# Kernel optimization log

Hardware: AMD Instinct MI355X
Metric: run time of the kernel (lower is better)

Reference implementation:

```python
import jax, jax.numpy as jnp
from jax import lax
import numpy as np

SEQ, BATCH, X_DIM = 256, 64, 64
FEAT = 256      # dense_x[-1]
DEC = 256       # dense_h_x[-1]
H = 512         # dim_rnn


def setup_inputs() -> dict:
    key = jax.random.key(0)
    ks = jax.random.split(key, 12)
    s = 0.05
    return {
        "x": jax.random.normal(ks[0], (SEQ, BATCH, X_DIM), jnp.float32),
        "mode_selector": jax.random.uniform(ks[1], (SEQ,), jnp.float32),
        # feature extractor: Linear(x_dim -> FEAT) + tanh
        "W_fx": jax.random.normal(ks[2], (FEAT, X_DIM), jnp.float32) * s,
        "b_fx": jnp.zeros((FEAT,), jnp.float32),
        # LSTM (single layer): gates ordered i, f, g, o (torch convention)
        "W_ih": jax.random.normal(ks[3], (4 * H, FEAT), jnp.float32) * s,
        "W_hh": jax.random.normal(ks[4], (4 * H, H), jnp.float32) * s,
        "b_ih": jnp.zeros((4 * H,), jnp.float32),
        "b_hh": jnp.zeros((4 * H,), jnp.float32),
        # decoder MLP: Linear(H -> DEC) + tanh
        "W_hx": jax.random.normal(ks[5], (DEC, H), jnp.float32) * s,
        "b_hx": jnp.zeros((DEC,), jnp.float32),
        # gen_out: Linear(DEC -> x_dim)
        "W_out": jax.random.normal(ks[6], (X_DIM, DEC), jnp.float32) * s,
        "b_out": jnp.zeros((X_DIM,), jnp.float32),
    }


def _forward(x, mode_selector, W_fx, b_fx, W_ih, W_hh, b_ih, b_hh,
             W_hx, b_hx, W_out, b_out):
    def fe(v):  # feature_extractor_x (dropout_p=0 -> identity)
        return jnp.tanh(v @ W_fx.T + b_fx)

    def gen(h):  # mlp_h_x + gen_out
        return jnp.tanh(h @ W_hx.T + b_hx) @ W_out.T + b_out

    def lstm_cell(feat, h, c):
        g = feat @ W_ih.T + b_ih + h @ W_hh.T + b_hh  # [B, 4H]
        i, f, gg, o = jnp.split(g, 4, axis=-1)
        c2 = jax.nn.sigmoid(f) * c + jax.nn.sigmoid(i) * jnp.tanh(gg)
        h2 = jax.nn.sigmoid(o) * jnp.tanh(c2)
        return h2, c2

    S, B, _ = x.shape
    feat_x = fe(x)  # [S, B, FEAT] teacher-forced features
    h0 = jnp.zeros((B, H), x.dtype)
    c0 = jnp.zeros((B, H), x.dtype)
    y0 = jnp.zeros((B, W_out.shape[0]), x.dtype)

    def step(carry, inp):
        h, c, y_prev = carry
        feat_tf, mix, is_first = inp
        # at t=0 original uses feature_x[0] as the "auto" feature
        feat_auto = jnp.where(is_first, feat_tf, fe(y_prev))
        feat = mix * feat_auto + (1.0 - mix) * feat_tf
        y_t = gen(h)           # generated from pre-update hidden state
        h2, c2 = lstm_cell(feat, h, c)
        return (h2, c2, y_t), y_t

    is_first = (jnp.arange(S) == 0)
    _, y = lax.scan(step, (h0, c0, y0), (feat_x, mode_selector, is_first))
    return y  # [S, B, x_dim]


def reference(x, mode_selector, W_fx, b_fx, W_ih, W_hh, b_ih, b_hh,
              W_hx, b_hx, W_out, b_out):
    return _forward(x, mode_selector, W_fx, b_fx, W_ih, W_hh, b_ih, b_hh,
                    W_hx, b_hx, W_out, b_out)
```

## Files before the change

### kernel.cpp

```cpp
#include <hip/hip_runtime.h>
#include <stdint.h>

typedef unsigned short u16;
typedef unsigned int u32;
typedef unsigned long long u64;
typedef __attribute__((ext_vector_type(8))) short short8;
typedef __attribute__((ext_vector_type(4))) float f32x4;
typedef __attribute__((ext_vector_type(4))) int int4v;

#define SEQ 256
#define GATE_WGS 64
#define D_WGS 8
#define NWG 73
#define A_ELE 49152
#define D_ELE 16384
#define FACC_ELE 16384

__device__ __forceinline__ u16 f2bf(float f) {
  u32 u = __float_as_uint(f);
  u += 0x7FFFu + ((u >> 16) & 1u);
  return (u16)(u >> 16);
}
__device__ __forceinline__ float bf2f(u16 v) {
  return __uint_as_float(((u32)v) << 16);
}
__device__ __forceinline__ short8 cvt8(const float* __restrict__ p) {
  short8 r;
#pragma unroll
  for (int j = 0; j < 8; ++j) r[j] = (short)f2bf(p[j]);
  return r;
}
__device__ __forceinline__ short8 cvt8v(const float* __restrict__ p) {
  f32x4 a = *(const f32x4*)p, b = *(const f32x4*)(p + 4);
  short8 r;
#pragma unroll
  for (int j = 0; j < 4; ++j) { r[j] = (short)f2bf(a[j]); r[4 + j] = (short)f2bf(b[j]); }
  return r;
}
__device__ __forceinline__ float fast_tanh(float x) {
  return 1.0f - 2.0f / (1.0f + __expf(2.0f * x));
}
__device__ __forceinline__ float fast_sig(float x) {
  return 1.0f / (1.0f + __expf(-x));
}

union V16 { short8 s; u64 q[2]; };
__device__ __forceinline__ short8 ldc16(const u16* p) {
  V16 v;
  v.q[0] = __hip_atomic_load((const u64*)p,     __ATOMIC_RELAXED, __HIP_MEMORY_SCOPE_AGENT);
  v.q[1] = __hip_atomic_load((const u64*)p + 1, __ATOMIC_RELAXED, __HIP_MEMORY_SCOPE_AGENT);
  return v.s;
}
__device__ __forceinline__ f32x4 ldc16f(const float* p) {
  union { f32x4 f; u64 q[2]; } v;
  v.q[0] = __hip_atomic_load((const u64*)p,     __ATOMIC_RELAXED, __HIP_MEMORY_SCOPE_AGENT);
  v.q[1] = __hip_atomic_load((const u64*)p + 1, __ATOMIC_RELAXED, __HIP_MEMORY_SCOPE_AGENT);
  return v.f;
}
__device__ __forceinline__ void stc16(u16* p, const u64* s) {
  __hip_atomic_store((u64*)p,     s[0], __ATOMIC_RELAXED, __HIP_MEMORY_SCOPE_AGENT);
  __hip_atomic_store((u64*)p + 1, s[1], __ATOMIC_RELAXED, __HIP_MEMORY_SCOPE_AGENT);
}
__device__ __forceinline__ void atadd(float* p, float v) {
  (void)__hip_atomic_fetch_add(p, v, __ATOMIC_RELAXED, __HIP_MEMORY_SCOPE_AGENT);
}
__device__ __forceinline__ void pollge(u32* p, u32 v) {
  while (__hip_atomic_load(p, __ATOMIC_RELAXED, __HIP_MEMORY_SCOPE_AGENT) < v) {}
}
__device__ __forceinline__ void setflag(u32* p, u32 v) {
  __hip_atomic_store(p, v, __ATOMIC_RELAXED, __HIP_MEMORY_SCOPE_AGENT);
}
#define VMCNT0() asm volatile("s_waitcnt vmcnt(0)" ::: "memory")

__global__ void prep_misc(const float* __restrict__ W_fx, const float* __restrict__ b_fx,
                          const float* __restrict__ W_out, const float* __restrict__ b_out,
                          u16* __restrict__ Abuf0, u32* __restrict__ flags,
                          float* __restrict__ featacc, float* __restrict__ bcomb,
                          u16* __restrict__ Wcpack) {
  int b = blockIdx.x, tid = threadIdx.x;
  if (b == 0) {
    for (int it = 0; it < 16; ++it) {
      int chunk = it * 256 + tid;
      *(int4v*)(Abuf0 + (2048 + chunk) * 8) = (int4v){0, 0, 0, 0};
    }
  } else if (b == 1) {
    for (int k = 0; k < 6; ++k) flags[k * 256 + tid] = 0u;
  } else if (b < 6) {
    float* base = featacc + (b - 2) * 16384;
    for (int it = 0; it < 16; ++it)
      *(f32x4*)(base + (it * 256 + tid) * 4) = (f32x4){0.f, 0.f, 0.f, 0.f};
  } else if (b == 6) {
    float s = b_fx[tid];
    for (int k = 0; k < 64; ++k) s += W_fx[tid * 64 + k] * b_out[k];
    bcomb[tid] = s;
  } else {
    int ct = b - 7;
    for (int it = 0; it < 16; ++it) {
      int o = it * 256 + tid;
      int cl = o >> 8, dec = o & 255;
      int c = ct * 16 + cl;
      float s = 0.f;
      for (int k = 0; k < 64; ++k) s += W_fx[c * 64 + k] * W_out[k * 256 + dec];
      int dw = dec >> 5, kd = dec & 31;
      int l = (c & 15) + ((kd >> 3) << 4), j = kd & 7;
      Wcpack[((dw * 16 + (c >> 4)) * 64 + l) * 8 + j] = f2bf(s);
    }
  }
}

__global__ void prep_ftf(const float* __restrict__ x, const float* __restrict__ W_fx,
                         const float* __restrict__ b_fx, u16* __restrict__ ftf) {
  __shared__ __attribute__((aligned(16))) u16 fstage[64 * 264];
  const int t = blockIdx.x, tid = threadIdx.x;
  const int wv = tid >> 6, ln = tid & 63;
  const int c15 = ln & 15, qq = ln >> 4;
  short8 WfR[2][4];
#pragma unroll
  for (int kk = 0; kk < 2; ++kk)
#pragma unroll
    for (int nt = 0; nt < 4; ++nt)
      WfR[kk][nt] = cvt8(W_fx + ((wv * 4 + nt) * 16 + c15) * 64 + kk * 32 + qq * 8);
  float bfx_r[4];
#pragma unroll
  for (int nt = 0; nt < 4; ++nt) bfx_r[nt] = b_fx[(wv * 4 + nt) * 16 + c15];
  short8 xa[2][4];
#pragma unroll
  for (int kb = 0; kb < 2; ++kb)
#pragma unroll
    for (int mt = 0; mt < 4; ++mt)
      xa[kb][mt] = cvt8v(x + (t * 64 + mt * 16 + c15) * 64 + kb * 32 + qq * 8);
  f32x4 tf[4][4];
#pragma unroll
  for (int nt = 0; nt < 4; ++nt)
#pragma unroll
    for (int mt = 0; mt < 4; ++mt) tf[nt][mt] = (f32x4){0.f, 0.f, 0.f, 0.f};
#pragma unroll
  for (int kb = 0; kb < 2; ++kb)
#pragma unroll
    for (int nt = 0; nt < 4; ++nt)
#pragma unroll
      for (int mt = 0; mt < 4; ++mt)
        tf[nt][mt] = __builtin_amdgcn_mfma_f32_16x16x32_bf16(xa[kb][mt], WfR[kb][nt], tf[nt][mt], 0, 0, 0);
#pragma unroll
  for (int nt = 0; nt < 4; ++nt)
#pragma unroll
    for (int mt = 0; mt < 4; ++mt)
#pragma unroll
      for (int r2 = 0; r2 < 4; ++r2) {
        int row = mt * 16 + qq * 4 + r2;
        fstage[row * 264 + (wv * 4 + nt) * 16 + c15] = f2bf(fast_tanh(tf[nt][mt][r2] + bfx_r[nt]));
      }
  __syncthreads();
  u16* ftfb = ftf + t * 16384;
#pragma unroll
  for (int it = 0; it < 8; ++it) {
    int chunk = it * 256 + tid;
    int kb = chunk >> 8, l = chunk & 63;
    int m = ((chunk >> 6) & 3) * 16 + (l & 15);
    int k = kb * 32 + (l >> 4) * 8;
    *(short8*)(ftfb + chunk * 8) = *(const short8*)(fstage + m * 264 + k);
  }
}

__global__ void __launch_bounds__(256, 1)
rnn_kernel(const float* __restrict__ x, const float* __restrict__ msel,
           const float* __restrict__ W_ih, const float* __restrict__ W_hh,
           const float* __restrict__ b_ih, const float* __restrict__ b_hh,
           const float* __restrict__ W_hx, const float* __restrict__ b_hx,
           const float* __restrict__ W_out, const float* __restrict__ b_out,
           float* __restrict__ out,
           u16* __restrict__ Abase, u16* __restrict__ dbase,
           u32* __restrict__ flags, float* __restrict__ featacc,
           const float* __restrict__ bcomb, const u16* __restrict__ Wcpack,
           const u16* __restrict__ ftf) {
  __shared__ __attribute__((aligned(16))) char smem[109568];
  const int wgid = blockIdx.x;
  const int tid = threadIdx.x;
  const int wv = tid >> 6, ln = tid & 63;
  u32* dflag = flags + 1024;
  u32* hcnt  = flags + 1168;
  u32* fcnt  = flags + 1232;

  if (wgid < GATE_WGS) {
    const int wg = wgid;
    float* red = (float*)smem;
    u16* hstage = (u16*)(smem + 32768);
    short8 Breg[6][2];
#pragma unroll
    for (int kk = 0; kk < 6; ++kk) {
      int kb = wv + kk * 4;
#pragma unroll
      for (int nt = 0; nt < 2; ++nt) {
        int n = ln & 15, q = ln >> 4;
        int gate = nt * 2 + (n >> 3), unit = n & 7;
        int row = gate * 512 + wg * 8 + unit;
        int k = kb * 32 + q * 8;
        const float* src = (k < 256) ? (W_ih + row * 256 + k) : (W_hh + row * 512 + (k - 256));
        Breg[kk][nt] = cvt8(src);
      }
    }
    float bcomb_r[2][8];
#pragma unroll
    for (int kk = 0; kk < 2; ++kk)
#pragma unroll
      for (int j = 0; j < 8; ++j)
        bcomb_r[kk][j] = bcomb[(wv + kk * 4) * 32 + (ln >> 4) * 8 + j];
    float bsum_r[2][4];
#pragma unroll
    for (int it = 0; it < 2; ++it) {
      int u = (it * 256 + tid) & 7;
#pragma unroll
      for (int g = 0; g < 4; ++g) {
        int row = g * 512 + wg * 8 + u;
        bsum_r[it][g] = b_ih[row] + b_hh[row];
      }
    }
    float creg[2] = {0.f, 0.f};
    const int kbW = 8 + (wg >> 2), qW = wg & 3;
    int r = 0, rn = 1;
    for (int t = 0; t < SEQ; ++t) {
      if (tid < 4) pollge(&hcnt[tid * 16], (u32)(16 * t));
      else if (tid == 64 && t > 0)
        pollge(&fcnt[((t - 1) & 3) * 16], 8u * (((u32)(t - 1) >> 2) + 1u));
      __syncthreads();
      const u16* A = Abase + r * A_ELE;
      u16* An = Abase + rn * A_ELE;
      short8 a[6][4];
#pragma unroll
      for (int kk = 2; kk < 6; ++kk) {
        int kb = wv + kk * 4;
#pragma unroll
        for (int mt = 0; mt < 4; ++mt)
          a[kk][mt] = ldc16(A + ((kb * 4 + mt) * 64 + ln) * 8);
      }
      const u16* ftfb = ftf + t * 16384;
      if (t == 0) {
#pragma unroll
        for (int kk = 0; kk < 2; ++kk) {
          int kb = wv + kk * 4;
#pragma unroll
          for (int mt = 0; mt < 4; ++mt)
            a[kk][mt] = *(const short8*)(ftfb + ((kb * 4 + mt) * 64 + ln) * 8);
        }
      } else {
        const float* fs = featacc + ((t - 1) & 3) * FACC_ELE;
        float mixg = msel[t];
#pragma unroll
        for (int kk = 0; kk < 2; ++kk) {
          int kb = wv + kk * 4;
#pragma unroll
          for (int mt = 0; mt < 4; ++mt) {
            int ch = (kb * 4 + mt) * 64 + ln;
            f32x4 lo = ldc16f(fs + ch * 8);
            f32x4 hi = ldc16f(fs + ch * 8 + 4);
            short8 tfv = *(const short8*)(ftfb + ch * 8);
            short8 rr;
#pragma unroll
            for (int j = 0; j < 8; ++j) {
              float av = ((j < 4) ? lo[j] : hi[j - 4]) + bcomb_r[kk][j];
              float fv = mixg * fast_tanh(av) + (1.f - mixg) * bf2f((u16)tfv[j]);
              rr[j] = (short)f2bf(fv);
            }
            a[kk][mt] = rr;
          }
        }
      }
      f32x4 acc[2][4];
#pragma unroll
      for (int nt = 0; nt < 2; nt++)
#pragma unroll
        for (int mt = 0; mt < 4; mt++) acc[nt][mt] = (f32x4){0.f, 0.f, 0.f, 0.f};
#pragma unroll
      for (int kk = 0; kk < 6; ++kk)
#pragma unroll
        for (int nt = 0; nt < 2; nt++)
#pragma unroll
          for (int mt = 0; mt < 4; mt++)
            acc[nt][mt] = __builtin_amdgcn_mfma_f32_16x16x32_bf16(a[kk][mt], Breg[kk][nt], acc[nt][mt], 0, 0, 0);
#pragma unroll
      for (int nt = 0; nt < 2; nt++)
#pragma unroll
        for (int mt = 0; mt < 4; mt++)
          *(f32x4*)(red + ((wv * 8 + nt * 4 + mt) * 64 + ln) * 4) = acc[nt][mt];
      __syncthreads();
#pragma unroll
      for (int it = 0; it < 2; ++it) {
        int item = it * 256 + tid;
        int m = item >> 3, u = item & 7;
        int mt = m >> 4, lq = ((m & 15) >> 2) * 16, reg = m & 3;
        float g4[4];
#pragma unroll
        for (int g = 0; g < 4; ++g) {
          float s = bsum_r[it][g];
          int base = ((g >> 1) * 4 + mt) * 64 + lq + (g & 1) * 8 + u;
#pragma unroll
          for (int w = 0; w < 4; ++w) s += red[(w * 8 * 64 + base) * 4 + reg];
          g4[g] = s;
        }
        float ii = fast_sig(g4[0]), ff = fast_sig(g4[1]);
        float gg = fast_tanh(g4[2]), oo = fast_sig(g4[3]);
        float cn = ff * creg[it] + ii * gg;
        creg[it] = cn;
        float h = oo * fast_tanh(cn);
        hstage[(mt * 16 + (m & 15)) * 8 + u] = f2bf(h);
      }
      __syncthreads();
      if (tid < 64) {
        u64 zq[2] = {0ull, 0ull};
        u16* fz = (u16*)featacc + ((t + 2) & 3) * 32768 + wg * 512 + tid * 8;
        stc16(fz, zq);
        int mt2 = tid >> 4, m15 = tid & 15;
        u16* dst = An + (((kbW * 4 + mt2) * 64 + qW * 16 + m15) * 8);
        stc16(dst, (const u64*)(hstage + tid * 8));
        VMCNT0();
        if (tid == 0)
          (void)__hip_atomic_fetch_add(&hcnt[(wg & 3) * 16], 1u,
                                       __ATOMIC_RELAXED, __HIP_MEMORY_SCOPE_AGENT);
      }
      r = rn; rn = (rn == 2) ? 0 : rn + 1;
    }
  } else if (wgid < GATE_WGS + D_WGS) {
    const int dw = wgid - GATE_WGS;
    float* red = (float*)smem;
    u16* dstage = (u16*)(smem + 32768);
    short8 Breg[4][2];
#pragma unroll
    for (int kk = 0; kk < 4; ++kk) {
      int kbh = wv * 4 + kk;
#pragma unroll
      for (int nt = 0; nt < 2; ++nt) {
        int n = ln & 15, q = ln >> 4;
        int row = dw * 32 + nt * 16 + n;
        int k = kbh * 32 + q * 8;
        Breg[kk][nt] = cvt8(W_hx + row * 512 + k);
      }
    }
    short8 WcB[4];
#pragma unroll
    for (int nt = 0; nt < 4; ++nt)
      WcB[nt] = *(const short8*)(Wcpack + ((dw * 16 + wv * 4 + nt) * 64 + ln) * 8);
    float bias_r[8];
#pragma unroll
    for (int it = 0; it < 8; ++it) bias_r[it] = b_hx[dw * 32 + ((it * 256 + tid) & 31)];
    int r = 0, rn = 1;
    for (int t = 0; t < SEQ; ++t) {
      if (tid < 4) pollge(&hcnt[tid * 16], (u32)(16 * t));
      __syncthreads();
      const u16* A = Abase + r * A_ELE;
      u16* dbufR = dbase + (t & 1) * D_ELE;
      short8 a[4][4];
#pragma unroll
      for (int kk = 0; kk < 4; ++kk)
#pragma unroll
        for (int mt = 0; mt < 4; ++mt)
          a[kk][mt] = ldc16(A + (((8 + wv * 4 + kk) * 4 + mt) * 64 + ln) * 8);
      f32x4 acc[2][4];
#pragma unroll
      for (int nt = 0; nt < 2; nt++)
#pragma unroll
        for (int mt = 0; mt < 4; mt++) acc[nt][mt] = (f32x4){0.f, 0.f, 0.f, 0.f};
#pragma unroll
      for (int kk = 0; kk < 4; ++kk)
#pragma unroll
        for (int nt = 0; nt < 2; nt++)
#pragma unroll
          for (int mt = 0; mt < 4; mt++)
            acc[nt][mt] = __builtin_amdgcn_mfma_f32_16x16x32_bf16(a[kk][mt], Breg[kk][nt], acc[nt][mt], 0, 0, 0);
#pragma unroll
      for (int nt = 0; nt < 2; nt++)
#pragma unroll
        for (int mt = 0; mt < 4; mt++)
          *(f32x4*)(red + ((wv * 8 + nt * 4 + mt) * 64 + ln) * 4) = acc[nt][mt];
      __syncthreads();
#pragma unroll
      for (int it = 0; it < 8; ++it) {
        int item = it * 256 + tid;
        int m = item >> 5, c = item & 31;
        int mt = m >> 4, lq = ((m & 15) >> 2) * 16, reg = m & 3;
        float s = bias_r[it];
        int base = ((c >> 4) * 4 + mt) * 64 + lq + (c & 15);
#pragma unroll
        for (int w = 0; w < 4; ++w) s += red[(w * 8 * 64 + base) * 4 + reg];
        dstage[((mt * 4 + (c >> 3)) * 16 + (m & 15)) * 8 + (c & 7)] = f2bf(fast_tanh(s));
      }
      __syncthreads();
      stc16(dbufR + (dw * 256 + tid) * 8, (const u64*)(dstage + tid * 8));
      short8 ad[4];
#pragma unroll
      for (int mt = 0; mt < 4; ++mt)
        ad[mt] = *(const short8*)(dstage + ((mt * 4 + (ln >> 4)) * 16 + (ln & 15)) * 8);
      f32x4 pacc[4][4];
#pragma unroll
      for (int nt = 0; nt < 4; ++nt)
#pragma unroll
        for (int mt = 0; mt < 4; ++mt) pacc[nt][mt] = (f32x4){0.f, 0.f, 0.f, 0.f};
#pragma unroll
      for (int nt = 0; nt < 4; ++nt)
#pragma unroll
        for (int mt = 0; mt < 4; ++mt)
          pacc[nt][mt] = __builtin_amdgcn_mfma_f32_16x16x32_bf16(ad[mt], WcB[nt], pacc[nt][mt], 0, 0, 0);
      {
        float* fs = featacc + (t & 3) * FACC_ELE;
#pragma unroll
        for (int nt = 0; nt < 4; ++nt) {
          int c = (wv * 4 + nt) * 16 + (ln & 15);
          int cb = (c >> 5) * 2048 + ((c & 31) >> 3) * 128 + (c & 7);
#pragma unroll
          for (int mt = 0; mt < 4; ++mt)
#pragma unroll
            for (int reg = 0; reg < 4; ++reg)
              atadd(fs + cb + mt * 512 + ((ln >> 4) * 4 + reg) * 8, pacc[nt][mt][reg]);
        }
      }
      VMCNT0();
      __syncthreads();
      if (tid == 0) {
        setflag(&dflag[dw * 16], (u32)(t + 1));
        (void)__hip_atomic_fetch_add(&fcnt[(t & 3) * 16], 1u,
                                     __ATOMIC_RELAXED, __HIP_MEMORY_SCOPE_AGENT);
      }
      r = rn; rn = (rn == 2) ? 0 : rn + 1;
    }
  } else {
    float* red = (float*)smem;
    const int c15 = ln & 15, qq = ln >> 4;
    short8 WoR[2][4];
#pragma unroll
    for (int kk = 0; kk < 2; ++kk) {
      int koffo = (wv * 2 + kk) * 32 + qq * 8;
#pragma unroll
      for (int nt = 0; nt < 4; ++nt)
        WoR[kk][nt] = cvt8(W_out + (nt * 16 + c15) * 256 + koffo);
    }
    float bout_r = b_out[wv * 16 + c15];
    for (int t = 0; t < SEQ; ++t) {
      if (tid < 8) pollge(&dflag[tid * 16], (u32)(t + 1));
      __syncthreads();
      const u16* dbufR = dbase + (t & 1) * D_ELE;
      short8 da[2][4];
#pragma unroll
      for (int kk = 0; kk < 2; ++kk)
#pragma unroll
        for (int mt = 0; mt < 4; ++mt)
          da[kk][mt] = ldc16(dbufR + (((wv * 2 + kk) * 4 + mt) * 64 + ln) * 8);
      f32x4 acc[4][4];
#pragma unroll
      for (int nt = 0; nt < 4; nt++)
#pragma unroll
        for (int mt = 0; mt < 4; mt++) acc[nt][mt] = (f32x4){0.f, 0.f, 0.f, 0.f};
#pragma unroll
      for (int kk = 0; kk < 2; ++kk)
#pragma unroll
        for (int nt = 0; nt < 4; nt++)
#pragma unroll
          for (int mt = 0; mt < 4; mt++)
            acc[nt][mt] = __builtin_amdgcn_mfma_f32_16x16x32_bf16(da[kk][mt], WoR[kk][nt], acc[nt][mt], 0, 0, 0);
#pragma unroll
      for (int nt = 0; nt < 4; nt++)
#pragma unroll
        for (int mt = 0; mt < 4; mt++)
          *(f32x4*)(red + ((wv * 16 + nt * 4 + mt) * 64 + ln) * 4) = acc[nt][mt];
      __syncthreads();
#pragma unroll
      for (int mt = 0; mt < 4; ++mt) {
        f32x4 s = (f32x4){0.f, 0.f, 0.f, 0.f};
#pragma unroll
        for (int w2 = 0; w2 < 4; ++w2)
          s += *(const f32x4*)(red + ((w2 * 16 + wv * 4 + mt) * 64 + ln) * 4);
#pragma unroll
        for (int r2 = 0; r2 < 4; ++r2) {
          int row = mt * 16 + qq * 4 + r2;
          out[t * 4096 + row * 64 + wv * 16 + c15] = s[r2] + bout_r;
        }
      }
      __syncthreads();
    }
  }
}

extern "C" void kernel_launch(void* const* d_in, const int* in_sizes, int n_in,
                              void* d_out, int out_size, void* d_ws, size_t ws_size,
                              hipStream_t stream) {
  const float* x     = (const float*)d_in[0];
  const float* msel  = (const float*)d_in[1];
  const float* W_fx  = (const float*)d_in[2];
  const float* b_fx  = (const float*)d_in[3];
  const float* W_ih  = (const float*)d_in[4];
  const float* W_hh  = (const float*)d_in[5];
  const float* b_ih  = (const float*)d_in[6];
  const float* b_hh  = (const float*)d_in[7];
  const float* W_hx  = (const float*)d_in[8];
  const float* b_hx  = (const float*)d_in[9];
  const float* W_out = (const float*)d_in[10];
  const float* b_out = (const float*)d_in[11];

  uint8_t* ws = (uint8_t*)d_ws;
  u16*   Abase   = (u16*)ws;
  u16*   dbase   = (u16*)(ws + 294912);
  u32*   flags   = (u32*)(ws + 360448);
  float* featacc = (float*)(ws + 368640);
  float* bcomb   = (float*)(ws + 630784);
  u16*   Wcpack  = (u16*)(ws + 631808);
  u16*   ftf     = (u16*)(ws + 762880);

  prep_misc<<<23, 256, 0, stream>>>(W_fx, b_fx, W_out, b_out,
                                    Abase, flags, featacc, bcomb, Wcpack);
  prep_ftf<<<256, 256, 0, stream>>>(x, W_fx, b_fx, ftf);
  rnn_kernel<<<NWG, 256, 0, stream>>>(x, msel, W_ih, W_hh, b_ih, b_hh,
                                      W_hx, b_hx, W_out, b_out,
                                      (float*)d_out, Abase, dbase, flags,
                                      featacc, bcomb, Wcpack, ftf);
}
```

Baseline: 2.221 ms.

## Replace atomic feature accumulation with per-decoder partial buffers and halve decoder workgroups

The decoder workgroups drop from 8 to 4, and each one now computes 64 output columns instead of 32. Each writes its partial product for the fed-back feature into its own slot with plain stores instead of float atomic adds into a shared accumulator. The gate workgroups then sum the four partials when they read the feature. This removes the atomic-add traffic, the per-step zeroing of the accumulator and the 4-deep ring, at the cost of four times the reads on the gate side, fewer parallel decoder workgroups and more work per decoder workgroup on the serial path.

```diff
diff --git a/kernel.cpp b/kernel.cpp
--- a/kernel.cpp
+++ b/kernel.cpp
@@ -10,11 +10,11 @@
 
 #define SEQ 256
 #define GATE_WGS 64
-#define D_WGS 8
-#define NWG 73
+#define D_WGS 4
+#define NWG 69
 #define A_ELE 49152
 #define D_ELE 16384
-#define FACC_ELE 16384
+#define FP_SLOT 65536
 
 __device__ __forceinline__ u16 f2bf(float f) {
   u32 u = __float_as_uint(f);
@@ -61,8 +61,8 @@
   __hip_atomic_store((u64*)p,     s[0], __ATOMIC_RELAXED, __HIP_MEMORY_SCOPE_AGENT);
   __hip_atomic_store((u64*)p + 1, s[1], __ATOMIC_RELAXED, __HIP_MEMORY_SCOPE_AGENT);
 }
-__device__ __forceinline__ void atadd(float* p, float v) {
-  (void)__hip_atomic_fetch_add(p, v, __ATOMIC_RELAXED, __HIP_MEMORY_SCOPE_AGENT);
+__device__ __forceinline__ void stc4f(float* p, float v) {
+  __hip_atomic_store((u32*)p, __float_as_uint(v), __ATOMIC_RELAXED, __HIP_MEMORY_SCOPE_AGENT);
 }
 __device__ __forceinline__ void pollge(u32* p, u32 v) {
   while (__hip_atomic_load(p, __ATOMIC_RELAXED, __HIP_MEMORY_SCOPE_AGENT) < v) {}
@@ -75,8 +75,7 @@
 __global__ void prep_misc(const float* __restrict__ W_fx, const float* __restrict__ b_fx,
                           const float* __restrict__ W_out, const float* __restrict__ b_out,
                           u16* __restrict__ Abuf0, u32* __restrict__ flags,
-                          float* __restrict__ featacc, float* __restrict__ bcomb,
-                          u16* __restrict__ Wcpack) {
+                          float* __restrict__ bcomb, u16* __restrict__ Wcpack) {
   int b = blockIdx.x, tid = threadIdx.x;
   if (b == 0) {
     for (int it = 0; it < 16; ++it) {
@@ -85,25 +84,21 @@
     }
   } else if (b == 1) {
     for (int k = 0; k < 6; ++k) flags[k * 256 + tid] = 0u;
-  } else if (b < 6) {
-    float* base = featacc + (b - 2) * 16384;
-    for (int it = 0; it < 16; ++it)
-      *(f32x4*)(base + (it * 256 + tid) * 4) = (f32x4){0.f, 0.f, 0.f, 0.f};
-  } else if (b == 6) {
+  } else if (b == 2) {
     float s = b_fx[tid];
     for (int k = 0; k < 64; ++k) s += W_fx[tid * 64 + k] * b_out[k];
     bcomb[tid] = s;
   } else {
-    int ct = b - 7;
+    int ct = b - 3;
     for (int it = 0; it < 16; ++it) {
       int o = it * 256 + tid;
       int cl = o >> 8, dec = o & 255;
       int c = ct * 16 + cl;
       float s = 0.f;
       for (int k = 0; k < 64; ++k) s += W_fx[c * 64 + k] * W_out[k * 256 + dec];
-      int dw = dec >> 5, kd = dec & 31;
+      int dwk = dec >> 5, kd = dec & 31;
       int l = (c & 15) + ((kd >> 3) << 4), j = kd & 7;
-      Wcpack[((dw * 16 + (c >> 4)) * 64 + l) * 8 + j] = f2bf(s);
+      Wcpack[((dwk * 16 + (c >> 4)) * 64 + l) * 8 + j] = f2bf(s);
     }
   }
 }
@@ -170,7 +165,7 @@
            const float* __restrict__ W_out, const float* __restrict__ b_out,
            float* __restrict__ out,
            u16* __restrict__ Abase, u16* __restrict__ dbase,
-           u32* __restrict__ flags, float* __restrict__ featacc,
+           u32* __restrict__ flags, float* __restrict__ fpart,
            const float* __restrict__ bcomb, const u16* __restrict__ Wcpack,
            const u16* __restrict__ ftf) {
   __shared__ __attribute__((aligned(16))) char smem[109568];
@@ -221,7 +216,7 @@
     for (int t = 0; t < SEQ; ++t) {
       if (tid < 4) pollge(&hcnt[tid * 16], (u32)(16 * t));
       else if (tid == 64 && t > 0)
-        pollge(&fcnt[((t - 1) & 3) * 16], 8u * (((u32)(t - 1) >> 2) + 1u));
+        pollge(&fcnt[((t - 1) & 1) * 16], 4u * ((((u32)(t - 1)) >> 1) + 1u));
       __syncthreads();
       const u16* A = Abase + r * A_ELE;
       u16* An = Abase + rn * A_ELE;
@@ -243,7 +238,7 @@
             a[kk][mt] = *(const short8*)(ftfb + ((kb * 4 + mt) * 64 + ln) * 8);
         }
       } else {
-        const float* fs = featacc + ((t - 1) & 3) * FACC_ELE;
+        const float* fp = fpart + ((t - 1) & 1) * FP_SLOT;
         float mixg = msel[t];
 #pragma unroll
         for (int kk = 0; kk < 2; ++kk) {
@@ -251,8 +246,13 @@
 #pragma unroll
           for (int mt = 0; mt < 4; ++mt) {
             int ch = (kb * 4 + mt) * 64 + ln;
-            f32x4 lo = ldc16f(fs + ch * 8);
-            f32x4 hi = ldc16f(fs + ch * 8 + 4);
+            f32x4 lo = ldc16f(fp + ch * 8);
+            f32x4 hi = ldc16f(fp + ch * 8 + 4);
+#pragma unroll
+            for (int dw = 1; dw < 4; ++dw) {
+              lo += ldc16f(fp + dw * 16384 + ch * 8);
+              hi += ldc16f(fp + dw * 16384 + ch * 8 + 4);
+            }
             short8 tfv = *(const short8*)(ftfb + ch * 8);
             short8 rr;
 #pragma unroll
@@ -306,9 +306,6 @@
       }
       __syncthreads();
       if (tid < 64) {
-        u64 zq[2] = {0ull, 0ull};
-        u16* fz = (u16*)featacc + ((t + 2) & 3) * 32768 + wg * 512 + tid * 8;
-        stc16(fz, zq);
         int mt2 = tid >> 4, m15 = tid & 15;
         u16* dst = An + (((kbW * 4 + mt2) * 64 + qW * 16 + m15) * 8);
         stc16(dst, (const u64*)(hstage + tid * 8));
@@ -322,26 +319,19 @@
   } else if (wgid < GATE_WGS + D_WGS) {
     const int dw = wgid - GATE_WGS;
     float* red = (float*)smem;
-    u16* dstage = (u16*)(smem + 32768);
-    short8 Breg[4][2];
-#pragma unroll
-    for (int kk = 0; kk < 4; ++kk) {
-      int kbh = wv * 4 + kk;
-#pragma unroll
-      for (int nt = 0; nt < 2; ++nt) {
-        int n = ln & 15, q = ln >> 4;
-        int row = dw * 32 + nt * 16 + n;
-        int k = kbh * 32 + q * 8;
+    u16* dstage = (u16*)(smem + 65536);
+    short8 Breg[4][4];
+#pragma unroll
+    for (int kk = 0; kk < 4; ++kk)
+#pragma unroll
+      for (int nt = 0; nt < 4; ++nt) {
+        int row = dw * 64 + nt * 16 + (ln & 15);
+        int k = (wv * 4 + kk) * 32 + (ln >> 4) * 8;
         Breg[kk][nt] = cvt8(W_hx + row * 512 + k);
       }
-    }
-    short8 WcB[4];
-#pragma unroll
-    for (int nt = 0; nt < 4; ++nt)
-      WcB[nt] = *(const short8*)(Wcpack + ((dw * 16 + wv * 4 + nt) * 64 + ln) * 8);
-    float bias_r[8];
-#pragma unroll
-    for (int it = 0; it < 8; ++it) bias_r[it] = b_hx[dw * 32 + ((it * 256 + tid) & 31)];
+    float bias_r[16];
+#pragma unroll
+    for (int it = 0; it < 16; ++it) bias_r[it] = b_hx[dw * 64 + ((it * 256 + tid) & 63)];
     int r = 0, rn = 1;
     for (int t = 0; t < SEQ; ++t) {
       if (tid < 4) pollge(&hcnt[tid * 16], (u32)(16 * t));
@@ -354,53 +344,65 @@
 #pragma unroll
         for (int mt = 0; mt < 4; ++mt)
           a[kk][mt] = ldc16(A + (((8 + wv * 4 + kk) * 4 + mt) * 64 + ln) * 8);
-      f32x4 acc[2][4];
-#pragma unroll
-      for (int nt = 0; nt < 2; nt++)
+      f32x4 acc[4][4];
+#pragma unroll
+      for (int nt = 0; nt < 4; nt++)
 #pragma unroll
         for (int mt = 0; mt < 4; mt++) acc[nt][mt] = (f32x4){0.f, 0.f, 0.f, 0.f};
 #pragma unroll
       for (int kk = 0; kk < 4; ++kk)
 #pragma unroll
-        for (int nt = 0; nt < 2; nt++)
+        for (int nt = 0; nt < 4; nt++)
 #pragma unroll
           for (int mt = 0; mt < 4; mt++)
             acc[nt][mt] = __builtin_amdgcn_mfma_f32_16x16x32_bf16(a[kk][mt], Breg[kk][nt], acc[nt][mt], 0, 0, 0);
 #pragma unroll
-      for (int nt = 0; nt < 2; nt++)
+      for (int nt = 0; nt < 4; nt++)
 #pragma unroll
         for (int mt = 0; mt < 4; mt++)
-          *(f32x4*)(red + ((wv * 8 + nt * 4 + mt) * 64 + ln) * 4) = acc[nt][mt];
-      __syncthreads();
-#pragma unroll
-      for (int it = 0; it < 8; ++it) {
+          *(f32x4*)(red + ((wv * 16 + nt * 4 + mt) * 64 + ln) * 4) = acc[nt][mt];
+      __syncthreads();
+#pragma unroll
+      for (int it = 0; it < 16; ++it) {
         int item = it * 256 + tid;
-        int m = item >> 5, c = item & 31;
-        int mt = m >> 4, lq = ((m & 15) >> 2) * 16, reg = m & 3;
+        int m = item >> 6, cloc = item & 63;
+        int mt = m >> 4, nt = cloc >> 4;
+        int lane = ((m & 15) >> 2) * 16 + (cloc & 15), reg = m & 3;
         float s = bias_r[it];
-        int base = ((c >> 4) * 4 + mt) * 64 + lq + (c & 15);
-#pragma unroll
-        for (int w = 0; w < 4; ++w) s += red[(w * 8 * 64 + base) * 4 + reg];
-        dstage[((mt * 4 + (c >> 3)) * 16 + (m & 15)) * 8 + (c & 7)] = f2bf(fast_tanh(s));
-      }
-      __syncthreads();
-      stc16(dbufR + (dw * 256 + tid) * 8, (const u64*)(dstage + tid * 8));
-      short8 ad[4];
-#pragma unroll
-      for (int mt = 0; mt < 4; ++mt)
-        ad[mt] = *(const short8*)(dstage + ((mt * 4 + (ln >> 4)) * 16 + (ln & 15)) * 8);
+#pragma unroll
+        for (int w = 0; w < 4; ++w) s += red[((w * 16 + nt * 4 + mt) * 64 + lane) * 4 + reg];
+        dstage[(((cloc >> 5) * 4 + mt) * 64 + ((cloc >> 3) & 3) * 16 + (m & 15)) * 8 + (cloc & 7)]
+            = f2bf(fast_tanh(s));
+      }
+      __syncthreads();
+#pragma unroll
+      for (int s2 = 0; s2 < 2; ++s2) {
+        int chunkl = s2 * 256 + tid;
+        stc16(dbufR + (dw * 512 + chunkl) * 8, (const u64*)(dstage + chunkl * 8));
+      }
+      short8 ad[2][4];
+#pragma unroll
+      for (int ks = 0; ks < 2; ++ks)
+#pragma unroll
+        for (int mt = 0; mt < 4; ++mt)
+          ad[ks][mt] = *(const short8*)(dstage + ((ks * 4 + mt) * 64 + ln) * 8);
       f32x4 pacc[4][4];
 #pragma unroll
       for (int nt = 0; nt < 4; ++nt)
 #pragma unroll
         for (int mt = 0; mt < 4; ++mt) pacc[nt][mt] = (f32x4){0.f, 0.f, 0.f, 0.f};
 #pragma unroll
-      for (int nt = 0; nt < 4; ++nt)
-#pragma unroll
-        for (int mt = 0; mt < 4; ++mt)
-          pacc[nt][mt] = __builtin_amdgcn_mfma_f32_16x16x32_bf16(ad[mt], WcB[nt], pacc[nt][mt], 0, 0, 0);
+      for (int ks = 0; ks < 2; ++ks) {
+#pragma unroll
+        for (int nt = 0; nt < 4; ++nt) {
+          short8 bw = *(const short8*)(Wcpack + (((dw * 2 + ks) * 16 + wv * 4 + nt) * 64 + ln) * 8);
+#pragma unroll
+          for (int mt = 0; mt < 4; ++mt)
+            pacc[nt][mt] = __builtin_amdgcn_mfma_f32_16x16x32_bf16(ad[ks][mt], bw, pacc[nt][mt], 0, 0, 0);
+        }
+      }
       {
-        float* fs = featacc + (t & 3) * FACC_ELE;
+        float* fpw = fpart + (t & 1) * FP_SLOT + dw * 16384;
 #pragma unroll
         for (int nt = 0; nt < 4; ++nt) {
           int c = (wv * 4 + nt) * 16 + (ln & 15);
@@ -409,14 +411,14 @@
           for (int mt = 0; mt < 4; ++mt)
 #pragma unroll
             for (int reg = 0; reg < 4; ++reg)
-              atadd(fs + cb + mt * 512 + ((ln >> 4) * 4 + reg) * 8, pacc[nt][mt][reg]);
+              stc4f(fpw + cb + mt * 512 + ((ln >> 4) * 4 + reg) * 8, pacc[nt][mt][reg]);
         }
       }
       VMCNT0();
       __syncthreads();
       if (tid == 0) {
         setflag(&dflag[dw * 16], (u32)(t + 1));
-        (void)__hip_atomic_fetch_add(&fcnt[(t & 3) * 16], 1u,
+        (void)__hip_atomic_fetch_add(&fcnt[(t & 1) * 16], 1u,
                                      __ATOMIC_RELAXED, __HIP_MEMORY_SCOPE_AGENT);
       }
       r = rn; rn = (rn == 2) ? 0 : rn + 1;
@@ -434,7 +436,7 @@
     }
     float bout_r = b_out[wv * 16 + c15];
     for (int t = 0; t < SEQ; ++t) {
-      if (tid < 8) pollge(&dflag[tid * 16], (u32)(t + 1));
+      if (tid < 4) pollge(&dflag[tid * 16], (u32)(t + 1));
       __syncthreads();
       const u16* dbufR = dbase + (t & 1) * D_ELE;
       short8 da[2][4];
@@ -495,19 +497,19 @@
   const float* b_out = (const float*)d_in[11];
 
   uint8_t* ws = (uint8_t*)d_ws;
-  u16*   Abase   = (u16*)ws;
-  u16*   dbase   = (u16*)(ws + 294912);
-  u32*   flags   = (u32*)(ws + 360448);
-  float* featacc = (float*)(ws + 368640);
-  float* bcomb   = (float*)(ws + 630784);
-  u16*   Wcpack  = (u16*)(ws + 631808);
-  u16*   ftf     = (u16*)(ws + 762880);
-
-  prep_misc<<<23, 256, 0, stream>>>(W_fx, b_fx, W_out, b_out,
-                                    Abase, flags, featacc, bcomb, Wcpack);
+  u16*   Abase  = (u16*)ws;
+  u16*   dbase  = (u16*)(ws + 294912);
+  u32*   flags  = (u32*)(ws + 360448);
+  float* fpart  = (float*)(ws + 368640);
+  float* bcomb  = (float*)(ws + 892928);
+  u16*   Wcpack = (u16*)(ws + 893952);
+  u16*   ftf    = (u16*)(ws + 1025024);
+
+  prep_misc<<<19, 256, 0, stream>>>(W_fx, b_fx, W_out, b_out,
+                                    Abase, flags, bcomb, Wcpack);
   prep_ftf<<<256, 256, 0, stream>>>(x, W_fx, b_fx, ftf);
   rnn_kernel<<<NWG, 256, 0, stream>>>(x, msel, W_ih, W_hh, b_ih, b_hh,
                                       W_hx, b_hx, W_out, b_out,
                                       (float*)d_out, Abase, dbase, flags,
-                                      featacc, bcomb, Wcpack, ftf);
-}
+                                      fpart, bcomb, Wcpack, ftf);
+}
```

After: 3.149 ms. 1.42x slower.

## Compute feature blend once in decoder workgroups instead of in every gate workgroup

Applied to the files above, without the earlier changes.

Previously each of the 64 gate workgroups read the full fp32 feature accumulator and redundantly applied bias, tanh and the teacher-forcing mix itself. Now the 8 decoder workgroups each blend a slice once per step into a double-buffered bf16 buffer, zero the accumulator, and signal a new counter. Gate workgroups then just load the ready bf16 features. This removes redundant global reads and transcendental work on the gate path, but adds an extra cross-workgroup synchronization hop on the recurrent critical path.

```diff
diff --git a/kernel.cpp b/kernel.cpp
--- a/kernel.cpp
+++ b/kernel.cpp
@@ -101,9 +101,9 @@
       int c = ct * 16 + cl;
       float s = 0.f;
       for (int k = 0; k < 64; ++k) s += W_fx[c * 64 + k] * W_out[k * 256 + dec];
-      int dw = dec >> 5, kd = dec & 31;
+      int dwk = dec >> 5, kd = dec & 31;
       int l = (c & 15) + ((kd >> 3) << 4), j = kd & 7;
-      Wcpack[((dw * 16 + (c >> 4)) * 64 + l) * 8 + j] = f2bf(s);
+      Wcpack[((dwk * 16 + (c >> 4)) * 64 + l) * 8 + j] = f2bf(s);
     }
   }
 }
@@ -172,7 +172,7 @@
            u16* __restrict__ Abase, u16* __restrict__ dbase,
            u32* __restrict__ flags, float* __restrict__ featacc,
            const float* __restrict__ bcomb, const u16* __restrict__ Wcpack,
-           const u16* __restrict__ ftf) {
+           const u16* __restrict__ ftf, u16* __restrict__ fblend) {
   __shared__ __attribute__((aligned(16))) char smem[109568];
   const int wgid = blockIdx.x;
   const int tid = threadIdx.x;
@@ -180,6 +180,7 @@
   u32* dflag = flags + 1024;
   u32* hcnt  = flags + 1168;
   u32* fcnt  = flags + 1232;
+  u32* fbcnt = flags + 1296;
 
   if (wgid < GATE_WGS) {
     const int wg = wgid;
@@ -199,12 +200,6 @@
         Breg[kk][nt] = cvt8(src);
       }
     }
-    float bcomb_r[2][8];
-#pragma unroll
-    for (int kk = 0; kk < 2; ++kk)
-#pragma unroll
-      for (int j = 0; j < 8; ++j)
-        bcomb_r[kk][j] = bcomb[(wv + kk * 4) * 32 + (ln >> 4) * 8 + j];
     float bsum_r[2][4];
 #pragma unroll
     for (int it = 0; it < 2; ++it) {
@@ -221,7 +216,7 @@
     for (int t = 0; t < SEQ; ++t) {
       if (tid < 4) pollge(&hcnt[tid * 16], (u32)(16 * t));
       else if (tid == 64 && t > 0)
-        pollge(&fcnt[((t - 1) & 3) * 16], 8u * (((u32)(t - 1) >> 2) + 1u));
+        pollge(&fbcnt[(t & 1) * 16], 8u * ((u32)(t + 1) >> 1));
       __syncthreads();
       const u16* A = Abase + r * A_ELE;
       u16* An = Abase + rn * A_ELE;
@@ -233,36 +228,14 @@
         for (int mt = 0; mt < 4; ++mt)
           a[kk][mt] = ldc16(A + ((kb * 4 + mt) * 64 + ln) * 8);
       }
-      const u16* ftfb = ftf + t * 16384;
-      if (t == 0) {
+      {
+        const u16* fsrc = (t == 0) ? ftf : (fblend + (t & 1) * 16384);
 #pragma unroll
         for (int kk = 0; kk < 2; ++kk) {
           int kb = wv + kk * 4;
 #pragma unroll
           for (int mt = 0; mt < 4; ++mt)
-            a[kk][mt] = *(const short8*)(ftfb + ((kb * 4 + mt) * 64 + ln) * 8);
-        }
-      } else {
-        const float* fs = featacc + ((t - 1) & 3) * FACC_ELE;
-        float mixg = msel[t];
-#pragma unroll
-        for (int kk = 0; kk < 2; ++kk) {
-          int kb = wv + kk * 4;
-#pragma unroll
-          for (int mt = 0; mt < 4; ++mt) {
-            int ch = (kb * 4 + mt) * 64 + ln;
-            f32x4 lo = ldc16f(fs + ch * 8);
-            f32x4 hi = ldc16f(fs + ch * 8 + 4);
-            short8 tfv = *(const short8*)(ftfb + ch * 8);
-            short8 rr;
-#pragma unroll
-            for (int j = 0; j < 8; ++j) {
-              float av = ((j < 4) ? lo[j] : hi[j - 4]) + bcomb_r[kk][j];
-              float fv = mixg * fast_tanh(av) + (1.f - mixg) * bf2f((u16)tfv[j]);
-              rr[j] = (short)f2bf(fv);
-            }
-            a[kk][mt] = rr;
-          }
+            a[kk][mt] = ldc16(fsrc + ((kb * 4 + mt) * 64 + ln) * 8);
         }
       }
       f32x4 acc[2][4];
@@ -306,9 +279,6 @@
       }
       __syncthreads();
       if (tid < 64) {
-        u64 zq[2] = {0ull, 0ull};
-        u16* fz = (u16*)featacc + ((t + 2) & 3) * 32768 + wg * 512 + tid * 8;
-        stc16(fz, zq);
         int mt2 = tid >> 4, m15 = tid & 15;
         u16* dst = An + (((kbW * 4 + mt2) * 64 + qW * 16 + m15) * 8);
         stc16(dst, (const u64*)(hstage + tid * 8));
@@ -342,6 +312,10 @@
     float bias_r[8];
 #pragma unroll
     for (int it = 0; it < 8; ++it) bias_r[it] = b_hx[dw * 32 + ((it * 256 + tid) & 31)];
+    const int ci = dw * 256 + tid;
+    const int cbase = (ci >> 8) * 32 + ((ci & 63) >> 4) * 8;
+    f32x4 bc0 = *(const f32x4*)(bcomb + cbase);
+    f32x4 bc1 = *(const f32x4*)(bcomb + cbase + 4);
     int r = 0, rn = 1;
     for (int t = 0; t < SEQ; ++t) {
       if (tid < 4) pollge(&hcnt[tid * 16], (u32)(16 * t));
@@ -418,6 +392,33 @@
         setflag(&dflag[dw * 16], (u32)(t + 1));
         (void)__hip_atomic_fetch_add(&fcnt[(t & 3) * 16], 1u,
                                      __ATOMIC_RELAXED, __HIP_MEMORY_SCOPE_AGENT);
+      }
+      if (t < SEQ - 1) {
+        if (tid == 0) pollge(&fcnt[(t & 3) * 16], 8u * (((u32)t >> 2) + 1u));
+        __syncthreads();
+        float* fs = featacc + (t & 3) * FACC_ELE;
+        f32x4 lo = ldc16f(fs + ci * 8);
+        f32x4 hi = ldc16f(fs + ci * 8 + 4);
+        short8 tfv = *(const short8*)(ftf + (t + 1) * 16384 + ci * 8);
+        float mixg = msel[t + 1];
+        VMCNT0();
+        short8 rr;
+#pragma unroll
+        for (int j = 0; j < 8; ++j) {
+          float av = ((j < 4) ? lo[j] : hi[j - 4]) + ((j < 4) ? bc0[j] : bc1[j - 4]);
+          float fv = mixg * fast_tanh(av) + (1.f - mixg) * bf2f((u16)tfv[j]);
+          rr[j] = (short)f2bf(fv);
+        }
+        V16 v; v.s = rr;
+        stc16(fblend + ((t + 1) & 1) * 16384 + ci * 8, v.q);
+        u64 zq[2] = {0ull, 0ull};
+        stc16((u16*)(fs + ci * 8), zq);
+        stc16((u16*)(fs + ci * 8 + 4), zq);
+        VMCNT0();
+        __syncthreads();
+        if (tid == 0)
+          (void)__hip_atomic_fetch_add(&fbcnt[((t + 1) & 1) * 16], 1u,
+                                       __ATOMIC_RELAXED, __HIP_MEMORY_SCOPE_AGENT);
       }
       r = rn; rn = (rn == 2) ? 0 : rn + 1;
     }
@@ -498,10 +499,11 @@
   u16*   Abase   = (u16*)ws;
   u16*   dbase   = (u16*)(ws + 294912);
   u32*   flags   = (u32*)(ws + 360448);
-  float* featacc = (float*)(ws + 368640);
-  float* bcomb   = (float*)(ws + 630784);
-  u16*   Wcpack  = (u16*)(ws + 631808);
-  u16*   ftf     = (u16*)(ws + 762880);
+  float* featacc = (float*)(ws + 366592);
+  float* bcomb   = (float*)(ws + 628736);
+  u16*   Wcpack  = (u16*)(ws + 629760);
+  u16*   fblend  = (u16*)(ws + 760832);
+  u16*   ftf     = (u16*)(ws + 826368);
 
   prep_misc<<<23, 256, 0, stream>>>(W_fx, b_fx, W_out, b_out,
                                     Abase, flags, featacc, bcomb, Wcpack);
@@ -509,5 +511,5 @@
   rnn_kernel<<<NWG, 256, 0, stream>>>(x, msel, W_ih, W_hh, b_ih, b_hh,
                                       W_hx, b_hx, W_out, b_out,
                                       (float*)d_out, Abase, dbase, flags,
-                                      featacc, bcomb, Wcpack, ftf);
-}
+                                      featacc, bcomb, Wcpack, ftf, fblend);
+}
```

Result: slower. 2.581 ms (+16.2%).
